# Kernel optimization log

Hardware: AMD Instinct MI355X
Metric: run time of the kernel (lower is better)

The kernel has to match this reference:

```python
import math
import jax, jax.numpy as jnp
import numpy as np

TAU = 2.0
THR = 1.0
ALPHA = 10.0

T, B, IN_DIM, OUT_DIM = 64, 128, 2048, 2048


def setup_inputs() -> dict:
    key = jax.random.key(0)
    k1, k2, k3 = jax.random.split(key, 3)
    x_seq = jax.random.normal(k1, (T, B, IN_DIM), dtype=jnp.float32)
    # scale like nn.Linear default init so membrane potentials are O(1)
    W = jax.random.normal(k2, (OUT_DIM, IN_DIM), dtype=jnp.float32) / math.sqrt(IN_DIM)
    b = jax.random.normal(k3, (OUT_DIM,), dtype=jnp.float32) * 0.01
    return {"x_seq": x_seq, "W": W, "b": b}


def spike(x):
    # forward: hard threshold (surrogate gradient only matters in bwd)
    return (x > 0).astype(x.dtype)


def reference(x_seq, W, b):
    decay = math.exp(-1.0 / TAU)
    # hoist the linear layer out of the recurrence: one big GEMM
    cur_seq = jnp.einsum("tbi,oi->tbo", x_seq, W) + b  # (T, B, OUT_DIM)
    mem0 = jnp.zeros((x_seq.shape[1], W.shape[0]), dtype=x_seq.dtype)

    def step(mem, cur):
        mem = mem * decay + cur
        spk = spike(mem - THR)
        mem = mem - spk * THR
        return mem, spk

    _, spk_seq = jax.lax.scan(step, mem0, cur_seq)
    return spk_seq  # (T, B, OUT_DIM)
```

## Files before the change

kernel.cpp:

```cpp
#include <hip/hip_runtime.h>
#include <hip/hip_bf16.h>
#include <math.h>


typedef unsigned short u16;
typedef __attribute__((ext_vector_type(8))) short bf16x8;
typedef __attribute__((ext_vector_type(4))) float f32x4;

constexpr int T_STEPS = 64;
constexpr int BATCH   = 128;
constexpr int K_DIM   = 2048;
constexpr int N_DIM   = 2048;
constexpr int M_DIM   = T_STEPS * BATCH;
constexpr int NCHAIN  = BATCH * N_DIM;

constexpr float DECAY_F32 = (float)0.6065306597126334;
constexpr float BAND      = 2e-4f;

#define GLDS16(g, l) __builtin_amdgcn_global_load_lds(                       \
    (const __attribute__((address_space(1))) void*)(g),                      \
    (__attribute__((address_space(3))) void*)(l), 16, 0, 0)

__global__ __launch_bounds__(256)
void split_bf16(const float* __restrict__ X, const float* __restrict__ W,
                u16* __restrict__ Ah, u16* __restrict__ Al,
                u16* __restrict__ Wh, u16* __restrict__ Wl,
                unsigned int* __restrict__ counters) {
    if (blockIdx.x == 0 && threadIdx.x < 128) counters[threadIdx.x] = 0u;

    constexpr int NA4 = (M_DIM * K_DIM) / 4;
    constexpr int NW4 = (N_DIM * K_DIM) / 4;
    const int i = blockIdx.x * 256 + threadIdx.x;
    const float* src; u16* dh; u16* dl; int base;
    if (i < NA4)            { src = X; dh = Ah; dl = Al; base = i; }
    else if (i < NA4 + NW4) { src = W; dh = Wh; dl = Wl; base = i - NA4; }
    else return;

    const float4 v = *(const float4*)(src + (size_t)base * 4);
    const float f[4] = {v.x, v.y, v.z, v.w};
    unsigned int hp[2], lp[2];
#pragma unroll
    for (int q = 0; q < 4; q += 2) {
        u16 hh[2], ll[2];
#pragma unroll
        for (int e = 0; e < 2; e++) {
            __hip_bfloat16 hb = __float2bfloat16(f[q + e]);
            const float hf = __bfloat162float(hb);
            __hip_bfloat16 lb = __float2bfloat16(f[q + e] - hf);
            hh[e] = *(u16*)&hb;
            ll[e] = *(u16*)&lb;
        }
        hp[q >> 1] = (unsigned int)hh[0] | ((unsigned int)hh[1] << 16);
        lp[q >> 1] = (unsigned int)ll[0] | ((unsigned int)ll[1] << 16);
    }
    *(uint2*)(dh + (size_t)base * 4) = make_uint2(hp[0], hp[1]);
    *(uint2*)(dl + (size_t)base * 4) = make_uint2(lp[0], lp[1]);
}

__global__ __launch_bounds__(512, 2)
void gemm_bf16x3p(const u16* __restrict__ Ah, const u16* __restrict__ Al,
                  const u16* __restrict__ Bh, const u16* __restrict__ Bl,
                  const float* __restrict__ bias, float* __restrict__ C) {
    extern __shared__ __align__(16) u16 smem[];
    u16* const sAh = smem;
    u16* const sAl = smem + 3 * 8192;
    u16* const sBh = smem + 6 * 8192;
    u16* const sBl = smem + 6 * 8192 + 3 * 4096;

    const int tid  = threadIdx.x;
    const int m0   = blockIdx.y * 256;
    const int n0   = blockIdx.x * 128;
    const int lane = tid & 63;
    const int wave = tid >> 6;
    const int wm   = wave >> 1;
    const int wn   = wave & 1;

    const int cA0 = tid, cA1 = tid + 512, cB0 = tid;
#define OFFA(c) ((size_t)(m0 + ((c) >> 6) * 16 + ((c) & 15)) * K_DIM + (((c) >> 4) & 3) * 8)
#define OFFB(c) ((size_t)(n0 + ((c) >> 6) * 16 + ((c) & 15)) * K_DIM + (((c) >> 4) & 3) * 8)
    const size_t a0 = OFFA(cA0), a1 = OFFA(cA1), b0 = OFFB(cB0);
#undef OFFA
#undef OFFB

    const int lA0 = wave * 512;
    const int lA1 = 4096 + wave * 512;
    const int lB0 = wave * 512;

    f32x4 acc[4][4];
#pragma unroll
    for (int i = 0; i < 4; i++)
#pragma unroll
        for (int j = 0; j < 4; j++) acc[i][j] = (f32x4){0.f, 0.f, 0.f, 0.f};

#define STAGE(s, kc) do {                                                    \
        const int kn_ = (kc) * 32;                                           \
        GLDS16(Ah + a0 + kn_, sAh + (s) * 8192 + lA0);                       \
        GLDS16(Ah + a1 + kn_, sAh + (s) * 8192 + lA1);                       \
        GLDS16(Al + a0 + kn_, sAl + (s) * 8192 + lA0);                       \
        GLDS16(Al + a1 + kn_, sAl + (s) * 8192 + lA1);                       \
        GLDS16(Bh + b0 + kn_, sBh + (s) * 4096 + lB0);                       \
        GLDS16(Bl + b0 + kn_, sBl + (s) * 4096 + lB0);                       \
    } while (0)

#define COMPUTE(rs) do {                                                     \
        bf16x8 fah[4], fal[4], fbh[4], fbl[4];                               \
        _Pragma("unroll")                                                    \
        for (int ti = 0; ti < 4; ti++) {                                     \
            const int ta = wm * 4 + ti;                                      \
            fah[ti] = *(const bf16x8*)&sAh[(rs) * 8192 + (ta * 64 + lane) * 8]; \
            fal[ti] = *(const bf16x8*)&sAl[(rs) * 8192 + (ta * 64 + lane) * 8]; \
        }                                                                    \
        _Pragma("unroll")                                                    \
        for (int tj = 0; tj < 4; tj++) {                                     \
            const int tb = wn * 4 + tj;                                      \
            fbh[tj] = *(const bf16x8*)&sBh[(rs) * 4096 + (tb * 64 + lane) * 8]; \
            fbl[tj] = *(const bf16x8*)&sBl[(rs) * 4096 + (tb * 64 + lane) * 8]; \
        }                                                                    \
        __builtin_amdgcn_s_setprio(1);                                       \
        _Pragma("unroll")                                                    \
        for (int ti = 0; ti < 4; ti++)                                       \
        _Pragma("unroll")                                                    \
        for (int tj = 0; tj < 4; tj++) {                                     \
            acc[ti][tj] = __builtin_amdgcn_mfma_f32_16x16x32_bf16(           \
                fah[ti], fbh[tj], acc[ti][tj], 0, 0, 0);                     \
            acc[ti][tj] = __builtin_amdgcn_mfma_f32_16x16x32_bf16(           \
                fah[ti], fbl[tj], acc[ti][tj], 0, 0, 0);                     \
            acc[ti][tj] = __builtin_amdgcn_mfma_f32_16x16x32_bf16(           \
                fal[ti], fbh[tj], acc[ti][tj], 0, 0, 0);                     \
        }                                                                    \
        __builtin_amdgcn_s_setprio(0);                                       \
    } while (0)

#define SYNC(vm) do {                                                        \
        asm volatile("s_waitcnt vmcnt(" #vm ")" ::: "memory");               \
        __builtin_amdgcn_sched_barrier(0);                                   \
        __builtin_amdgcn_s_barrier();                                        \
        __builtin_amdgcn_sched_barrier(0);                                   \
    } while (0)

    STAGE(0, 0);
    STAGE(1, 1);

    for (int kcb = 0; kcb < 63; kcb += 3) {
        SYNC(6);
        STAGE(2, kcb + 2);
        COMPUTE(0);
        SYNC(6);
        STAGE(0, kcb + 3);
        COMPUTE(1);
        SYNC(6);
        if (kcb + 4 < 64) STAGE(1, kcb + 4);
        COMPUTE(2);
    }
    SYNC(0);
    COMPUTE(0);

#undef SYNC
#undef COMPUTE
#undef STAGE

#pragma unroll
    for (int tj = 0; tj < 4; tj++) {
        const int n  = n0 + wn * 64 + tj * 16 + (lane & 15);
        const float bv = bias[n];
#pragma unroll
        for (int ti = 0; ti < 4; ti++) {
            const int mbase = m0 + wm * 64 + ti * 16 + (lane >> 4) * 4;
#pragma unroll
            for (int r = 0; r < 4; r++)
                C[(size_t)(mbase + r) * N_DIM + n] = acc[ti][tj][r] + bv;
        }
    }
}

__global__ __launch_bounds__(256)
void lif_scan_band(float* __restrict__ buf, unsigned int* __restrict__ counters,
                   unsigned int* __restrict__ worklist) {
    const int idx = blockIdx.x * 256 + threadIdx.x;
    float mem = 0.0f;
    bool flag = false;
#pragma unroll
    for (int t = 0; t < T_STEPS; t++) {
        const size_t off = (size_t)t * NCHAIN + idx;
        mem = __fadd_rn(__fmul_rn(mem, DECAY_F32), buf[off]);
        const float d = __fsub_rn(mem, 1.0f);
        const bool spk = d > 0.0f;
        if (fabsf(d) < BAND) flag = true;
        buf[off] = spk ? 1.0f : 0.0f;
        if (spk) mem = __fsub_rn(mem, 1.0f);
    }
    if (flag) {
        const int b = idx >> 11, o = idx & 2047;
        const unsigned int p = atomicAdd(&counters[b], 1u);
        worklist[b * 2048 + p] = (unsigned int)o;
    }
}

#define RG 16
#define RJ 4
#define BKR 64

__global__ __launch_bounds__(256)
void lif_repair2(const float* __restrict__ X, const float* __restrict__ W,
                 const float* __restrict__ bias,
                 const unsigned int* __restrict__ counters,
                 const unsigned int* __restrict__ worklist,
                 float* __restrict__ out) {
    __shared__ float sX[BKR][T_STEPS + 1];
    __shared__ float sW[RG][BKR + 1];
    __shared__ float scur[T_STEPS][RG + 1];
    __shared__ float sspk[T_STEPS][RG + 1];
    __shared__ int   so[RG];

    const int b = blockIdx.x / RJ;
    const int j = blockIdx.x % RJ;
    const unsigned int n_b = counters[b];
    if (n_b == 0) return;
    const int ngroups = (int)(n_b + RG - 1) / RG;

    const int tid = threadIdx.x;
    const int t   = tid & 63;
    const int oi  = tid >> 6;

    for (int g = j; g < ngroups; g += RJ) {
        if (tid < RG) {
            const int slot = g * RG + tid;
            so[tid] = (slot < (int)n_b) ? (int)worklist[b * 2048 + slot] : -1;
        }
        __syncthreads();

        float Csum[4] = {0.f, 0.f, 0.f, 0.f};
        float P[4]    = {0.f, 0.f, 0.f, 0.f};

        for (int c = 0; c < K_DIM / BKR; c++) {
            if (c > 0 && (c % 5) == 0) {
#pragma unroll
                for (int q = 0; q < 4; q++) {
                    Csum[q] = __fadd_rn(Csum[q], P[q]);
                    P[q] = 0.f;
                }
            }
            const int k0 = c * BKR;
            {
                const int ts = tid >> 2;
                const int kq = (tid & 3) * 16;
                const float* src = &X[(size_t)(ts * BATCH + b) * K_DIM + k0 + kq];
#pragma unroll
                for (int q = 0; q < 4; q++) {
                    const float4 v = *(const float4*)(src + q * 4);
                    sX[kq + q * 4 + 0][ts] = v.x;
                    sX[kq + q * 4 + 1][ts] = v.y;
                    sX[kq + q * 4 + 2][ts] = v.z;
                    sX[kq + q * 4 + 3][ts] = v.w;
                }
            }
            {
                const int wo  = tid >> 4;
                const int wkq = (tid & 15) * 4;
                const int o   = so[wo];
                float4 v = {0.f, 0.f, 0.f, 0.f};
                if (o >= 0) v = *(const float4*)&W[(size_t)o * K_DIM + k0 + wkq];
                sW[wo][wkq + 0] = v.x; sW[wo][wkq + 1] = v.y;
                sW[wo][wkq + 2] = v.z; sW[wo][wkq + 3] = v.w;
            }
            __syncthreads();
#pragma unroll 8
            for (int k = 0; k < BKR; k++) {
                const float xv = sX[k][t];
#pragma unroll
                for (int q = 0; q < 4; q++)
                    P[q] = fmaf(xv, sW[oi * 4 + q][k], P[q]);
            }
            __syncthreads();
        }
#pragma unroll
        for (int q = 0; q < 4; q++) {
            Csum[q] = __fadd_rn(Csum[q], P[q]);
            const int o = so[oi * 4 + q];
            scur[t][oi * 4 + q] = (o >= 0) ? __fadd_rn(Csum[q], bias[o]) : 0.f;
        }
        __syncthreads();
        if (tid < RG && so[tid] >= 0) {
            float mem = 0.0f;
            for (int tt = 0; tt < T_STEPS; tt++) {
                mem = __fadd_rn(__fmul_rn(mem, DECAY_F32), scur[tt][tid]);
                const float d = __fsub_rn(mem, 1.0f);
                const bool spk = d > 0.0f;
                sspk[tt][tid] = spk ? 1.0f : 0.0f;
                if (spk) mem = __fsub_rn(mem, 1.0f);
            }
        }
        __syncthreads();
#pragma unroll
        for (int q = 0; q < 4; q++) {
            const int o = so[oi * 4 + q];
            if (o >= 0)
                out[(size_t)t * NCHAIN + (size_t)b * N_DIM + o] = sspk[t][oi * 4 + q];
        }
        __syncthreads();
    }
}

__global__ __launch_bounds__(256)
void lif_openblas_q320(const float* __restrict__ X, const float* __restrict__ W,
                       const float* __restrict__ bias, float* __restrict__ out) {
    __shared__ float As[16][T_STEPS + 4];
    __shared__ float Ws[16][64 + 4];
    __shared__ float curbuf[T_STEPS][64 + 1];
    const int tid = threadIdx.x;
    const int o0 = blockIdx.x * 64, b0 = blockIdx.y;
    const int tm = (tid & 15) * 4, tn = (tid >> 4) * 4;
    float Csum[4][4], Pacc[4][4];
#pragma unroll
    for (int i = 0; i < 4; i++)
#pragma unroll
        for (int j = 0; j < 4; j++) { Csum[i][j] = 0.f; Pacc[i][j] = 0.f; }
    for (int c = 0; c < K_DIM / 16; c++) {
        if (c > 0 && (c % 20) == 0) {
#pragma unroll
            for (int i = 0; i < 4; i++)
#pragma unroll
                for (int j = 0; j < 4; j++) {
                    Csum[i][j] = __fadd_rn(Csum[i][j], Pacc[i][j]);
                    Pacc[i][j] = 0.f;
                }
        }
        const int k0 = c * 16;
        {
            const int t = tid >> 2, kq = (tid & 3) * 4;
            const float4 av = *(const float4*)&X[(size_t)(t * BATCH + b0) * K_DIM + k0 + kq];
            As[kq + 0][t] = av.x; As[kq + 1][t] = av.y;
            As[kq + 2][t] = av.z; As[kq + 3][t] = av.w;
            const float4 wv = *(const float4*)&W[(size_t)(o0 + t) * K_DIM + k0 + kq];
            Ws[kq + 0][t] = wv.x; Ws[kq + 1][t] = wv.y;
            Ws[kq + 2][t] = wv.z; Ws[kq + 3][t] = wv.w;
        }
        __syncthreads();
#pragma unroll
        for (int k = 0; k < 16; k++) {
            float a[4], w[4];
#pragma unroll
            for (int i = 0; i < 4; i++) a[i] = As[k][tm + i];
#pragma unroll
            for (int j = 0; j < 4; j++) w[j] = Ws[k][tn + j];
#pragma unroll
            for (int i = 0; i < 4; i++)
#pragma unroll
                for (int j = 0; j < 4; j++) Pacc[i][j] = fmaf(a[i], w[j], Pacc[i][j]);
        }
        __syncthreads();
    }
#pragma unroll
    for (int i = 0; i < 4; i++)
#pragma unroll
        for (int j = 0; j < 4; j++)
            curbuf[tm + i][tn + j] =
                __fadd_rn(__fadd_rn(Csum[i][j], Pacc[i][j]), bias[o0 + tn + j]);
    __syncthreads();
    if (tid < 64) {
        float mem = 0.0f;
#pragma unroll
        for (int t = 0; t < T_STEPS; t++) {
            mem = __fadd_rn(__fmul_rn(mem, DECAY_F32), curbuf[t][tid]);
            const float d = __fsub_rn(mem, 1.0f);
            const bool spk = d > 0.0f;
            out[(size_t)t * NCHAIN + (size_t)b0 * N_DIM + o0 + tid] = spk ? 1.0f : 0.0f;
            if (spk) mem = __fsub_rn(mem, 1.0f);
        }
    }
}

extern "C" void kernel_launch(void* const* d_in, const int* in_sizes, int n_in,
                              void* d_out, int out_size, void* d_ws, size_t ws_size,
                              hipStream_t stream) {
    const float* x = nullptr; const float* W = nullptr; const float* bias = nullptr;
    for (int i = 0; i < n_in; i++) {
        if      (in_sizes[i] == M_DIM * K_DIM) x    = (const float*)d_in[i];
        else if (in_sizes[i] == N_DIM * K_DIM) W    = (const float*)d_in[i];
        else if (in_sizes[i] == N_DIM)         bias = (const float*)d_in[i];
    }
    if (!x)    x    = (const float*)d_in[0];
    if (!W)    W    = (const float*)d_in[1];
    if (!bias) bias = (const float*)d_in[2];
    float* out = (float*)d_out;

    const size_t off_cnt = 0;
    const size_t off_wl  = 512;
    const size_t off_Ah  = off_wl + (size_t)128 * 2048 * 4;
    const size_t szA     = (size_t)M_DIM * K_DIM * 2;
    const size_t szW     = (size_t)N_DIM * K_DIM * 2;
    const size_t off_Al  = off_Ah + szA;
    const size_t off_Wh  = off_Al + szA;
    const size_t off_Wl  = off_Wh + szW;
    const size_t need    = off_Wl + szW;

    if (ws_size < need) {
        dim3 grid(N_DIM / 64, BATCH);
        lif_openblas_q320<<<grid, 256, 0, stream>>>(x, W, bias, out);
        return;
    }

    char* ws = (char*)d_ws;
    unsigned int* counters = (unsigned int*)(ws + off_cnt);
    unsigned int* worklist = (unsigned int*)(ws + off_wl);
    u16* Ah = (u16*)(ws + off_Ah);
    u16* Al = (u16*)(ws + off_Al);
    u16* Wh = (u16*)(ws + off_Wh);
    u16* Wl = (u16*)(ws + off_Wl);

    split_bf16<<<(M_DIM * K_DIM / 4 + N_DIM * K_DIM / 4) / 256, 256, 0, stream>>>(
        x, W, Ah, Al, Wh, Wl, counters);
    dim3 ggrid(N_DIM / 128, M_DIM / 256);
    gemm_bf16x3p<<<ggrid, 512, 147456, stream>>>(Ah, Al, Wh, Wl, bias, out);
    lif_scan_band<<<NCHAIN / 256, 256, 0, stream>>>(out, counters, worklist);
    lif_repair2<<<128 * RJ, 256, 0, stream>>>(x, W, bias, counters, worklist, out);
}
```

Measured before the change: 470.7 us.

## Widen split and scan memory accesses and remap GEMM tiles across XCDs

The bf16 split kernel now handles 8 floats per thread with 16-byte stores, and the LIF scan processes 4 neuron chains per thread using float4 loads and stores. The GEMM remaps its workgroup index so that consecutive tiles land on the same XCD (chiplet), aiming for better L2 reuse of the A and B operands. These changes target memory-bound stages and cache locality. In exchange, the scan launches fewer threads, which lowers occupancy for latency hiding, and the tile remap assumes a fixed grid of 16x32 blocks.

```diff
diff --git a/kernel.cpp b/kernel.cpp
--- a/kernel.cpp
+++ b/kernel.cpp
@@ -28,19 +28,20 @@
                 unsigned int* __restrict__ counters) {
     if (blockIdx.x == 0 && threadIdx.x < 128) counters[threadIdx.x] = 0u;
 
-    constexpr int NA4 = (M_DIM * K_DIM) / 4;
-    constexpr int NW4 = (N_DIM * K_DIM) / 4;
+    constexpr int NA8 = (M_DIM * K_DIM) / 8;
+    constexpr int NW8 = (N_DIM * K_DIM) / 8;
     const int i = blockIdx.x * 256 + threadIdx.x;
     const float* src; u16* dh; u16* dl; int base;
-    if (i < NA4)            { src = X; dh = Ah; dl = Al; base = i; }
-    else if (i < NA4 + NW4) { src = W; dh = Wh; dl = Wl; base = i - NA4; }
+    if (i < NA8)            { src = X; dh = Ah; dl = Al; base = i; }
+    else if (i < NA8 + NW8) { src = W; dh = Wh; dl = Wl; base = i - NA8; }
     else return;
 
-    const float4 v = *(const float4*)(src + (size_t)base * 4);
-    const float f[4] = {v.x, v.y, v.z, v.w};
-    unsigned int hp[2], lp[2];
-#pragma unroll
-    for (int q = 0; q < 4; q += 2) {
+    const float4 v0 = *(const float4*)(src + (size_t)base * 8);
+    const float4 v1 = *(const float4*)(src + (size_t)base * 8 + 4);
+    const float f[8] = {v0.x, v0.y, v0.z, v0.w, v1.x, v1.y, v1.z, v1.w};
+    unsigned int hp[4], lp[4];
+#pragma unroll
+    for (int q = 0; q < 8; q += 2) {
         u16 hh[2], ll[2];
 #pragma unroll
         for (int e = 0; e < 2; e++) {
@@ -53,8 +54,8 @@
         hp[q >> 1] = (unsigned int)hh[0] | ((unsigned int)hh[1] << 16);
         lp[q >> 1] = (unsigned int)ll[0] | ((unsigned int)ll[1] << 16);
     }
-    *(uint2*)(dh + (size_t)base * 4) = make_uint2(hp[0], hp[1]);
-    *(uint2*)(dl + (size_t)base * 4) = make_uint2(lp[0], lp[1]);
+    *(uint4*)(dh + (size_t)base * 8) = make_uint4(hp[0], hp[1], hp[2], hp[3]);
+    *(uint4*)(dl + (size_t)base * 8) = make_uint4(lp[0], lp[1], lp[2], lp[3]);
 }
 
 __global__ __launch_bounds__(512, 2)
@@ -68,8 +69,10 @@
     u16* const sBl = smem + 6 * 8192 + 3 * 4096;
 
     const int tid  = threadIdx.x;
-    const int m0   = blockIdx.y * 256;
-    const int n0   = blockIdx.x * 128;
+    const int orig = blockIdx.x + gridDim.x * blockIdx.y;
+    const int wg   = (orig & 7) * 64 + (orig >> 3);
+    const int m0   = (wg >> 4) * 256;
+    const int n0   = (wg & 15) * 128;
     const int lane = tid & 63;
     const int wave = tid >> 6;
     const int wm   = wave >> 1;
@@ -174,25 +177,35 @@
 }
 
 __global__ __launch_bounds__(256)
-void lif_scan_band(float* __restrict__ buf, unsigned int* __restrict__ counters,
-                   unsigned int* __restrict__ worklist) {
-    const int idx = blockIdx.x * 256 + threadIdx.x;
-    float mem = 0.0f;
-    bool flag = false;
+void lif_scan_band4(float* __restrict__ buf, unsigned int* __restrict__ counters,
+                    unsigned int* __restrict__ worklist) {
+    const int idx = (blockIdx.x * 256 + threadIdx.x) * 4;
+    float mem[4]  = {0.f, 0.f, 0.f, 0.f};
+    bool  flag[4] = {false, false, false, false};
 #pragma unroll
     for (int t = 0; t < T_STEPS; t++) {
         const size_t off = (size_t)t * NCHAIN + idx;
-        mem = __fadd_rn(__fmul_rn(mem, DECAY_F32), buf[off]);
-        const float d = __fsub_rn(mem, 1.0f);
-        const bool spk = d > 0.0f;
-        if (fabsf(d) < BAND) flag = true;
-        buf[off] = spk ? 1.0f : 0.0f;
-        if (spk) mem = __fsub_rn(mem, 1.0f);
-    }
-    if (flag) {
-        const int b = idx >> 11, o = idx & 2047;
-        const unsigned int p = atomicAdd(&counters[b], 1u);
-        worklist[b * 2048 + p] = (unsigned int)o;
+        const float4 v = *(const float4*)(buf + off);
+        const float c[4] = {v.x, v.y, v.z, v.w};
+        float s[4];
+#pragma unroll
+        for (int q = 0; q < 4; q++) {
+            mem[q] = __fadd_rn(__fmul_rn(mem[q], DECAY_F32), c[q]);
+            const float d = __fsub_rn(mem[q], 1.0f);
+            const bool spk = d > 0.0f;
+            if (fabsf(d) < BAND) flag[q] = true;
+            s[q] = spk ? 1.0f : 0.0f;
+            if (spk) mem[q] = __fsub_rn(mem[q], 1.0f);
+        }
+        *(float4*)(buf + off) = make_float4(s[0], s[1], s[2], s[3]);
+    }
+    const int b = idx >> 11;
+#pragma unroll
+    for (int q = 0; q < 4; q++) {
+        if (flag[q]) {
+            const unsigned int p = atomicAdd(&counters[b], 1u);
+            worklist[b * 2048 + p] = (unsigned int)((idx + q) & 2047);
+        }
     }
 }
 
@@ -408,10 +421,10 @@
     u16* Wh = (u16*)(ws + off_Wh);
     u16* Wl = (u16*)(ws + off_Wl);
 
-    split_bf16<<<(M_DIM * K_DIM / 4 + N_DIM * K_DIM / 4) / 256, 256, 0, stream>>>(
+    split_bf16<<<(M_DIM * K_DIM / 8 + N_DIM * K_DIM / 8) / 256, 256, 0, stream>>>(
         x, W, Ah, Al, Wh, Wl, counters);
     dim3 ggrid(N_DIM / 128, M_DIM / 256);
     gemm_bf16x3p<<<ggrid, 512, 147456, stream>>>(Ah, Al, Wh, Wl, bias, out);
-    lif_scan_band<<<NCHAIN / 256, 256, 0, stream>>>(out, counters, worklist);
+    lif_scan_band4<<<NCHAIN / 1024, 256, 0, stream>>>(out, counters, worklist);
     lif_repair2<<<128 * RJ, 256, 0, stream>>>(x, W, bias, counters, worklist, out);
 }
```

Result: faster. 456.9 us (-2.9%).
